# Kernel tuning notes

Hardware: AMD Instinct MI355X
Metric: run time of the kernel (lower is better)

Reference implementation:

```python
import jax, jax.numpy as jnp
import numpy as np
from jax import lax

B, C, D, H, W = 2, 64, 64, 96, 96
HID = 8  # max(C // 8, 8)
NEG_SLOPE = 0.01  # torch LeakyReLU default


def setup_inputs() -> dict:
    key = jax.random.key(0)
    k_x, k_dw, k_f1w, k_f1b, k_f2w, k_f2b = jax.random.split(key, 6)
    x = jax.random.normal(k_x, (B, C, D, H, W), dtype=jnp.float32)
    # depthwise 3x3x3 kernel, OIDHW with I = C/groups = 1
    dw_w = jax.random.normal(k_dw, (C, 1, 3, 3, 3), dtype=jnp.float32) * 0.2
    fc1_w = jax.random.normal(k_f1w, (HID, C), dtype=jnp.float32) * 0.1
    fc1_b = jax.random.normal(k_f1b, (HID,), dtype=jnp.float32) * 0.1
    fc2_w = jax.random.normal(k_f2w, (C, HID), dtype=jnp.float32) * 0.1
    fc2_b = jax.random.normal(k_f2b, (C,), dtype=jnp.float32) * 0.1
    return {"x": x, "dw_w": dw_w, "fc1_w": fc1_w, "fc1_b": fc1_b,
            "fc2_w": fc2_w, "fc2_b": fc2_b}


def reference(x, dw_w, fc1_w, fc1_b, fc2_w, fc2_b):
    # depthwise 3x3x3 conv, padding=1, groups=C
    s = lax.conv_general_dilated(
        x, dw_w,
        window_strides=(1, 1, 1),
        padding=[(1, 1), (1, 1), (1, 1)],
        dimension_numbers=("NCDHW", "OIDHW", "NCDHW"),
        feature_group_count=C,
    )
    # squeeze: global average pool over D,H,W -> [B, C]
    z = s.mean(axis=(2, 3, 4))
    # excitation MLP (1x1x1 convs on [B,C,1,1,1] == dense layers on [B,C])
    h = jnp.einsum("bc,hc->bh", z, fc1_w) + fc1_b
    h = jnp.where(h >= 0, h, NEG_SLOPE * h)  # LeakyReLU(0.01)
    w = jax.nn.sigmoid(jnp.einsum("bh,ch->bc", h, fc2_w) + fc2_b)
    # broadcast channel gate
    return x * w[:, :, None, None, None]
```

## Files before the change

kernel.cpp:

```cpp
#include <hip/hip_runtime.h>
#include <math.h>

#define B 2
#define C 64
#define DD 64
#define HH 96
#define WW 96
#define HID 8
#define BC (B * C)
#define SLICE (HH * WW)
#define SLICE4 (SLICE / 4)
#define CHAN (DD * SLICE)
#define CHAN4 (CHAN / 4)
#define ROW4 (WW / 4)

#define RED_BX 16
#define DPB (DD / RED_BX)
#define SC_F4 16
#define SC_BX (CHAN4 / (256 * SC_F4))

#define WS_PART 0
#define WS_CLS  (BC * RED_BX)
#define WS_GATE (WS_CLS + C * 27)

typedef float f4 __attribute__((ext_vector_type(4)));

__global__ void clsw_kernel(const float* __restrict__ dw_w, float* __restrict__ ws) {
    int c = blockIdx.x;
    int t = threadIdx.x;
    if (t < 27) {
        int cd = t / 9, r = t % 9, ch = r / 3, cw = r % 3;
        int kd0 = (cd == 2) ? 1 : 0, kd1 = (cd == 0) ? 1 : 2;
        int kh0 = (ch == 2) ? 1 : 0, kh1 = (ch == 0) ? 1 : 2;
        int kw0 = (cw == 2) ? 1 : 0, kw1 = (cw == 0) ? 1 : 2;
        float s = 0.f;
        for (int kd = kd0; kd <= kd1; ++kd)
            for (int kh = kh0; kh <= kh1; ++kh)
                for (int kw = kw0; kw <= kw1; ++kw)
                    s += dw_w[c * 27 + kd * 9 + kh * 3 + kw];
        ws[WS_CLS + c * 27 + t] = s;
    }
}

__global__ __launch_bounds__(256) void reduce_kernel(const float* __restrict__ x,
                                                     float* __restrict__ ws) {
    const int bc = blockIdx.y;
    const int c  = bc & (C - 1);
    const int d0 = blockIdx.x * DPB;
    const int tid = threadIdx.x;

    __shared__ float w9[9];
    __shared__ float part[4];

    const f4* xb = (const f4*)x + (size_t)bc * CHAN4;
    float acc = 0.f;

    const int h0 = tid / ROW4;
    const int j0 = tid - h0 * ROW4;

    for (int sd = 0; sd < DPB; ++sd) {
        const int d  = d0 + sd;
        const int cd = (d == 0) ? 0 : ((d == DD - 1) ? 2 : 1);
        __syncthreads();
        if (tid < 9) w9[tid] = ws[WS_CLS + c * 27 + cd * 9 + tid];
        __syncthreads();

        const f4* x4 = xb + (size_t)d * SLICE4;
        int h = h0, j = j0;
        #pragma unroll
        for (int it = 0; it < SLICE4 / 256; ++it) {
            f4 v = x4[it * 256 + tid];
            int chc = (h == 0) ? 0 : ((h == HH - 1) ? 2 : 1);
            float wmid = w9[chc * 3 + 1];
            float w0 = (j == 0) ? w9[chc * 3 + 0] : wmid;
            float w3 = (j == ROW4 - 1) ? w9[chc * 3 + 2] : wmid;
            acc += v.x * w0 + (v.y + v.z) * wmid + v.w * w3;
            h += 10; j += 16;
            if (j >= ROW4) { j -= ROW4; h += 1; }
        }
    }

    for (int off = 32; off > 0; off >>= 1)
        acc += __shfl_down(acc, off, 64);
    if ((tid & 63) == 0) part[tid >> 6] = acc;
    __syncthreads();
    if (tid == 0)
        ws[WS_PART + bc * RED_BX + blockIdx.x] = part[0] + part[1] + part[2] + part[3];
}

__global__ void gate_kernel(const float* __restrict__ fc1_w, const float* __restrict__ fc1_b,
                            const float* __restrict__ fc2_w, const float* __restrict__ fc2_b,
                            float* __restrict__ ws) {
    __shared__ float zsh[BC];
    __shared__ float hsh[B * HID];
    int t = threadIdx.x;
    float s0 = 0.f;
    for (int p = 0; p < RED_BX; ++p) s0 += ws[WS_PART + t * RED_BX + p];
    zsh[t] = s0 * (1.0f / (float)CHAN);
    __syncthreads();
    if (t < B * HID) {
        int b = t >> 3, j = t & 7;
        float s = fc1_b[j];
        for (int cc = 0; cc < C; ++cc) s += fc1_w[j * C + cc] * zsh[b * C + cc];
        hsh[t] = (s >= 0.f) ? s : 0.01f * s;
    }
    __syncthreads();
    int b = t >> 6, cc = t & (C - 1);
    float s = fc2_b[cc];
    for (int j = 0; j < HID; ++j) s += fc2_w[cc * HID + j] * hsh[b * HID + j];
    ws[WS_GATE + t] = 1.f / (1.f + expf(-s));
}

__global__ __launch_bounds__(256) void scale_kernel(const float* __restrict__ x,
                                                    const float* __restrict__ ws,
                                                    float* __restrict__ out) {
    const int bc = blockIdx.y;
    const float g = ws[WS_GATE + bc];
    const size_t base = (size_t)bc * CHAN4 + (size_t)blockIdx.x * (256 * SC_F4) + threadIdx.x;
    const f4* xp = (const f4*)x;
    f4* op = (f4*)out;
    #pragma unroll
    for (int k = 0; k < SC_F4; ++k) {
        size_t idx = base + (size_t)k * 256;
        f4 v = __builtin_nontemporal_load(&xp[idx]);
        f4 r = v * g;
        __builtin_nontemporal_store(r, &op[idx]);
    }
}

extern "C" void kernel_launch(void* const* d_in, const int* in_sizes, int n_in,
                              void* d_out, int out_size, void* d_ws, size_t ws_size,
                              hipStream_t stream) {
    const float* x     = (const float*)d_in[0];
    const float* dw_w  = (const float*)d_in[1];
    const float* fc1_w = (const float*)d_in[2];
    const float* fc1_b = (const float*)d_in[3];
    const float* fc2_w = (const float*)d_in[4];
    const float* fc2_b = (const float*)d_in[5];
    float* out = (float*)d_out;
    float* ws  = (float*)d_ws;

    clsw_kernel<<<dim3(C), dim3(64), 0, stream>>>(dw_w, ws);
    reduce_kernel<<<dim3(RED_BX, BC), dim3(256), 0, stream>>>(x, ws);
    gate_kernel<<<dim3(1), dim3(BC), 0, stream>>>(fc1_w, fc1_b, fc2_w, fc2_b, ws);
    scale_kernel<<<dim3(SC_BX, BC), dim3(256), 0, stream>>>(x, ws, out);
}
```

Before: 544.6 us.

## Fuse SE reduce, gate and scale into one cooperative persistent kernel

Replaces the four-kernel pipeline with a single cooperative kernel of 1024 blocks. Each block reduces its slab of x for both batches, waits at a grid-wide sync, computes the gate redundantly, then rescales the same slab in reverse order so the most recently read data may still be in cache. Edge-weight precompute moves into each block, and a non-cooperative fallback path is kept. This is meant to remove launch gaps and the second full read of x from HBM, at the cost of a grid barrier, redundant gate MLP work per block, and an occupancy requirement for co-residency.

```diff
diff --git a/kernel.cpp b/kernel.cpp
--- a/kernel.cpp
+++ b/kernel.cpp
@@ -1,4 +1,5 @@
 #include <hip/hip_runtime.h>
+#include <hip/hip_cooperative_groups.h>
 #include <math.h>
 
 #define B 2
@@ -14,22 +15,21 @@
 #define CHAN4 (CHAN / 4)
 #define ROW4 (WW / 4)
 
-#define RED_BX 16
-#define DPB (DD / RED_BX)
-#define SC_F4 16
-#define SC_BX (CHAN4 / (256 * SC_F4))
+#define NCHUNK 16
+#define DPB (DD / NCHUNK)
+#define GRID_BLK 1024
+#define ITERS (DPB * SLICE4 / 256)
 
 #define WS_PART 0
-#define WS_CLS  (BC * RED_BX)
-#define WS_GATE (WS_CLS + C * 27)
+#define WS_GATE (BC * NCHUNK)
 
 typedef float f4 __attribute__((ext_vector_type(4)));
-
-__global__ void clsw_kernel(const float* __restrict__ dw_w, float* __restrict__ ws) {
-    int c = blockIdx.x;
-    int t = threadIdx.x;
-    if (t < 27) {
-        int cd = t / 9, r = t % 9, ch = r / 3, cw = r % 3;
+namespace cg = cooperative_groups;
+
+__device__ __forceinline__ void compute_clsw(const float* __restrict__ dw_w,
+                                             int c, int tid, float* w27) {
+    if (tid < 27) {
+        int cd = tid / 9, r = tid % 9, ch = r / 3, cw = r % 3;
         int kd0 = (cd == 2) ? 1 : 0, kd1 = (cd == 0) ? 1 : 2;
         int kh0 = (ch == 2) ? 1 : 0, kh1 = (ch == 0) ? 1 : 2;
         int kw0 = (cw == 2) ? 1 : 0, kw1 = (cw == 0) ? 1 : 2;
@@ -38,34 +38,20 @@
             for (int kh = kh0; kh <= kh1; ++kh)
                 for (int kw = kw0; kw <= kw1; ++kw)
                     s += dw_w[c * 27 + kd * 9 + kh * 3 + kw];
-        ws[WS_CLS + c * 27 + t] = s;
-    }
-}
-
-__global__ __launch_bounds__(256) void reduce_kernel(const float* __restrict__ x,
-                                                     float* __restrict__ ws) {
-    const int bc = blockIdx.y;
-    const int c  = bc & (C - 1);
-    const int d0 = blockIdx.x * DPB;
-    const int tid = threadIdx.x;
-
-    __shared__ float w9[9];
-    __shared__ float part[4];
-
-    const f4* xb = (const f4*)x + (size_t)bc * CHAN4;
+        w27[tid] = s;
+    }
+}
+
+__device__ __forceinline__ float reduce_task(const float* __restrict__ x,
+                                             const float* w27,
+                                             int bc, int d0, int tid,
+                                             int h0, int j0) {
+    const f4* xb = (const f4*)x + (size_t)bc * CHAN4 + (size_t)d0 * SLICE4;
     float acc = 0.f;
-
-    const int h0 = tid / ROW4;
-    const int j0 = tid - h0 * ROW4;
-
     for (int sd = 0; sd < DPB; ++sd) {
-        const int d  = d0 + sd;
-        const int cd = (d == 0) ? 0 : ((d == DD - 1) ? 2 : 1);
-        __syncthreads();
-        if (tid < 9) w9[tid] = ws[WS_CLS + c * 27 + cd * 9 + tid];
-        __syncthreads();
-
-        const f4* x4 = xb + (size_t)d * SLICE4;
+        const int d = d0 + sd;
+        const float* w9 = &w27[((d == 0) ? 0 : ((d == DD - 1) ? 2 : 1)) * 9];
+        const f4* x4 = xb + (size_t)sd * SLICE4;
         int h = h0, j = j0;
         #pragma unroll
         for (int it = 0; it < SLICE4 / 256; ++it) {
@@ -79,23 +65,117 @@
             if (j >= ROW4) { j -= ROW4; h += 1; }
         }
     }
-
-    for (int off = 32; off > 0; off >>= 1)
-        acc += __shfl_down(acc, off, 64);
-    if ((tid & 63) == 0) part[tid >> 6] = acc;
-    __syncthreads();
-    if (tid == 0)
-        ws[WS_PART + bc * RED_BX + blockIdx.x] = part[0] + part[1] + part[2] + part[3];
-}
-
-__global__ void gate_kernel(const float* __restrict__ fc1_w, const float* __restrict__ fc1_b,
-                            const float* __restrict__ fc2_w, const float* __restrict__ fc2_b,
-                            float* __restrict__ ws) {
+    return acc;
+}
+
+__global__ __launch_bounds__(256, 4) void fused_se(
+        const float* __restrict__ x, const float* __restrict__ dw_w,
+        const float* __restrict__ fc1_w, const float* __restrict__ fc1_b,
+        const float* __restrict__ fc2_w, const float* __restrict__ fc2_b,
+        float* __restrict__ out, float* __restrict__ ws) {
+    const int tid   = threadIdx.x;
+    const int c     = blockIdx.x >> 4;
+    const int chunk = blockIdx.x & (NCHUNK - 1);
+    const int d0    = chunk * DPB;
+
+    __shared__ float w27[27];
+    __shared__ float part[4];
+    __shared__ float zsh[BC];
+    __shared__ float hsh[B * HID];
+    __shared__ float gsh[BC];
+
+    compute_clsw(dw_w, c, tid, w27);
+    __syncthreads();
+
+    const int h0 = tid / ROW4;
+    const int j0 = tid - h0 * ROW4;
+
+    for (int sel = 0; sel < 2; ++sel) {
+        const int bc = sel * C + c;
+        float acc = reduce_task(x, w27, bc, d0, tid, h0, j0);
+        for (int off = 32; off > 0; off >>= 1)
+            acc += __shfl_down(acc, off, 64);
+        __syncthreads();
+        if ((tid & 63) == 0) part[tid >> 6] = acc;
+        __syncthreads();
+        if (tid == 0)
+            ws[WS_PART + bc * NCHUNK + chunk] = part[0] + part[1] + part[2] + part[3];
+    }
+
+    __threadfence();
+    cg::this_grid().sync();
+
+    if (tid < BC) {
+        float s0 = 0.f;
+        #pragma unroll
+        for (int p = 0; p < NCHUNK; ++p) s0 += ws[WS_PART + tid * NCHUNK + p];
+        zsh[tid] = s0 * (1.0f / (float)CHAN);
+    }
+    __syncthreads();
+    if (tid < B * HID) {
+        int b = tid >> 3, j = tid & 7;
+        float s = fc1_b[j];
+        for (int cc = 0; cc < C; ++cc) s += fc1_w[j * C + cc] * zsh[b * C + cc];
+        hsh[tid] = (s >= 0.f) ? s : 0.01f * s;
+    }
+    __syncthreads();
+    if (tid < BC) {
+        int b = tid >> 6, cc = tid & (C - 1);
+        float s = fc2_b[cc];
+        for (int j = 0; j < HID; ++j) s += fc2_w[cc * HID + j] * hsh[b * HID + j];
+        gsh[tid] = 1.f / (1.f + expf(-s));
+    }
+    __syncthreads();
+
+    const f4* xp = (const f4*)x;
+    f4* op = (f4*)out;
+    for (int sel = 1; sel >= 0; --sel) {
+        const int bc = sel * C + c;
+        const float g = gsh[bc];
+        const size_t base = (size_t)bc * CHAN4 + (size_t)d0 * SLICE4 + tid;
+        #pragma unroll 6
+        for (int it = ITERS - 1; it >= 0; --it) {
+            size_t idx = base + (size_t)it * 256;
+            f4 v = xp[idx];
+            __builtin_nontemporal_store(v * g, &op[idx]);
+        }
+    }
+}
+
+__global__ __launch_bounds__(256) void fb_reduce(const float* __restrict__ x,
+                                                 const float* __restrict__ dw_w,
+                                                 float* __restrict__ ws) {
+    const int tid   = threadIdx.x;
+    const int c     = blockIdx.x >> 4;
+    const int chunk = blockIdx.x & (NCHUNK - 1);
+    const int d0    = chunk * DPB;
+    __shared__ float w27[27];
+    __shared__ float part[4];
+    compute_clsw(dw_w, c, tid, w27);
+    __syncthreads();
+    const int h0 = tid / ROW4;
+    const int j0 = tid - h0 * ROW4;
+    for (int sel = 0; sel < 2; ++sel) {
+        const int bc = sel * C + c;
+        float acc = reduce_task(x, w27, bc, d0, tid, h0, j0);
+        for (int off = 32; off > 0; off >>= 1)
+            acc += __shfl_down(acc, off, 64);
+        __syncthreads();
+        if ((tid & 63) == 0) part[tid >> 6] = acc;
+        __syncthreads();
+        if (tid == 0)
+            ws[WS_PART + bc * NCHUNK + chunk] = part[0] + part[1] + part[2] + part[3];
+    }
+}
+
+__global__ void fb_gate(const float* __restrict__ fc1_w, const float* __restrict__ fc1_b,
+                        const float* __restrict__ fc2_w, const float* __restrict__ fc2_b,
+                        float* __restrict__ ws) {
     __shared__ float zsh[BC];
     __shared__ float hsh[B * HID];
     int t = threadIdx.x;
     float s0 = 0.f;
-    for (int p = 0; p < RED_BX; ++p) s0 += ws[WS_PART + t * RED_BX + p];
+    for (int p = 0; p < NCHUNK; ++p) s0 += ws[WS_PART + t * NCHUNK + p];
     zsh[t] = s0 * (1.0f / (float)CHAN);
     __syncthreads();
     if (t < B * HID) {
@@ -111,20 +191,25 @@
     ws[WS_GATE + t] = 1.f / (1.f + expf(-s));
 }
 
-__global__ __launch_bounds__(256) void scale_kernel(const float* __restrict__ x,
-                                                    const float* __restrict__ ws,
-                                                    float* __restrict__ out) {
-    const int bc = blockIdx.y;
-    const float g = ws[WS_GATE + bc];
-    const size_t base = (size_t)bc * CHAN4 + (size_t)blockIdx.x * (256 * SC_F4) + threadIdx.x;
+__global__ __launch_bounds__(256) void fb_scale(const float* __restrict__ x,
+                                                const float* __restrict__ ws,
+                                                float* __restrict__ out) {
+    const int tid   = threadIdx.x;
+    const int c     = blockIdx.x >> 4;
+    const int chunk = blockIdx.x & (NCHUNK - 1);
+    const int d0    = chunk * DPB;
     const f4* xp = (const f4*)x;
     f4* op = (f4*)out;
-    #pragma unroll
-    for (int k = 0; k < SC_F4; ++k) {
-        size_t idx = base + (size_t)k * 256;
-        f4 v = __builtin_nontemporal_load(&xp[idx]);
-        f4 r = v * g;
-        __builtin_nontemporal_store(r, &op[idx]);
+    for (int sel = 1; sel >= 0; --sel) {
+        const int bc = sel * C + c;
+        const float g = ws[WS_GATE + bc];
+        const size_t base = (size_t)bc * CHAN4 + (size_t)d0 * SLICE4 + tid;
+        #pragma unroll 6
+        for (int it = ITERS - 1; it >= 0; --it) {
+            size_t idx = base + (size_t)it * 256;
+            f4 v = xp[idx];
+            __builtin_nontemporal_store(v * g, &op[idx]);
+        }
     }
 }
 
@@ -140,8 +225,13 @@
     float* out = (float*)d_out;
     float* ws  = (float*)d_ws;
 
-    clsw_kernel<<<dim3(C), dim3(64), 0, stream>>>(dw_w, ws);
-    reduce_kernel<<<dim3(RED_BX, BC), dim3(256), 0, stream>>>(x, ws);
-    gate_kernel<<<dim3(1), dim3(BC), 0, stream>>>(fc1_w, fc1_b, fc2_w, fc2_b, ws);
-    scale_kernel<<<dim3(SC_BX, BC), dim3(256), 0, stream>>>(x, ws, out);
-}
+    void* args[] = {(void*)&x, (void*)&dw_w, (void*)&fc1_w, (void*)&fc1_b,
+                    (void*)&fc2_w, (void*)&fc2_b, (void*)&out, (void*)&ws};
+    hipError_t e = hipLaunchCooperativeKernel(
+        reinterpret_cast<void*>(fused_se), dim3(GRID_BLK), dim3(256), args, 0, stream);
+    if (e != hipSuccess) {
+        fb_reduce<<<dim3(GRID_BLK), dim3(256), 0, stream>>>(x, dw_w, ws);
+        fb_gate<<<dim3(1), dim3(BC), 0, stream>>>(fc1_w, fc1_b, fc2_w, fc2_b, ws);
+        fb_scale<<<dim3(GRID_BLK), dim3(256), 0, stream>>>(x, ws, out);
+    }
+}
```

After: 863.8 us. +58.6%, slower.

## Fold weight-sum kernel into reduce, reverse scale order for cache reuse

Applied to the files above, without the earlier changes.

Removes the separate clsw kernel launch by having each reduce block compute the 27 boundary-class weight sums into shared memory once, which also drops the per-slice syncthreads pairs. The scale kernel now walks channels and blocks in reverse order and uses normal loads and stores instead of nontemporal ones. The intent is for the tail of x read last by the reduce pass to still be in the large last-level cache when scale starts. The cost is a redundant weight-sum computation in every reduce block and possible cache pollution from the ordinary stores.

```diff
diff --git a/kernel.cpp b/kernel.cpp
--- a/kernel.cpp
+++ b/kernel.cpp
@@ -20,16 +20,14 @@
 #define SC_BX (CHAN4 / (256 * SC_F4))
 
 #define WS_PART 0
-#define WS_CLS  (BC * RED_BX)
-#define WS_GATE (WS_CLS + C * 27)
+#define WS_GATE (BC * RED_BX)
 
 typedef float f4 __attribute__((ext_vector_type(4)));
 
-__global__ void clsw_kernel(const float* __restrict__ dw_w, float* __restrict__ ws) {
-    int c = blockIdx.x;
-    int t = threadIdx.x;
-    if (t < 27) {
-        int cd = t / 9, r = t % 9, ch = r / 3, cw = r % 3;
+__device__ __forceinline__ void compute_clsw(const float* __restrict__ dw_w,
+                                             int c, int tid, float* w27) {
+    if (tid < 27) {
+        int cd = tid / 9, r = tid % 9, ch = r / 3, cw = r % 3;
         int kd0 = (cd == 2) ? 1 : 0, kd1 = (cd == 0) ? 1 : 2;
         int kh0 = (ch == 2) ? 1 : 0, kh1 = (ch == 0) ? 1 : 2;
         int kw0 = (cw == 2) ? 1 : 0, kw1 = (cw == 0) ? 1 : 2;
@@ -38,19 +36,23 @@
             for (int kh = kh0; kh <= kh1; ++kh)
                 for (int kw = kw0; kw <= kw1; ++kw)
                     s += dw_w[c * 27 + kd * 9 + kh * 3 + kw];
-        ws[WS_CLS + c * 27 + t] = s;
+        w27[tid] = s;
     }
 }
 
 __global__ __launch_bounds__(256) void reduce_kernel(const float* __restrict__ x,
+                                                     const float* __restrict__ dw_w,
                                                      float* __restrict__ ws) {
     const int bc = blockIdx.y;
     const int c  = bc & (C - 1);
     const int d0 = blockIdx.x * DPB;
     const int tid = threadIdx.x;
 
-    __shared__ float w9[9];
+    __shared__ float w27[27];
     __shared__ float part[4];
+
+    compute_clsw(dw_w, c, tid, w27);
+    __syncthreads();
 
     const f4* xb = (const f4*)x + (size_t)bc * CHAN4;
     float acc = 0.f;
@@ -60,11 +62,7 @@
 
     for (int sd = 0; sd < DPB; ++sd) {
         const int d  = d0 + sd;
-        const int cd = (d == 0) ? 0 : ((d == DD - 1) ? 2 : 1);
-        __syncthreads();
-        if (tid < 9) w9[tid] = ws[WS_CLS + c * 27 + cd * 9 + tid];
-        __syncthreads();
-
+        const float* w9 = &w27[((d == 0) ? 0 : ((d == DD - 1) ? 2 : 1)) * 9];
         const f4* x4 = xb + (size_t)d * SLICE4;
         int h = h0, j = j0;
         #pragma unroll
@@ -114,17 +112,16 @@
 __global__ __launch_bounds__(256) void scale_kernel(const float* __restrict__ x,
                                                     const float* __restrict__ ws,
                                                     float* __restrict__ out) {
-    const int bc = blockIdx.y;
+    const int bc = (BC - 1) - blockIdx.y;
+    const int bx = (SC_BX - 1) - blockIdx.x;
     const float g = ws[WS_GATE + bc];
-    const size_t base = (size_t)bc * CHAN4 + (size_t)blockIdx.x * (256 * SC_F4) + threadIdx.x;
+    const size_t base = (size_t)bc * CHAN4 + (size_t)bx * (256 * SC_F4) + threadIdx.x;
     const f4* xp = (const f4*)x;
     f4* op = (f4*)out;
     #pragma unroll
     for (int k = 0; k < SC_F4; ++k) {
         size_t idx = base + (size_t)k * 256;
-        f4 v = __builtin_nontemporal_load(&xp[idx]);
-        f4 r = v * g;
-        __builtin_nontemporal_store(r, &op[idx]);
+        op[idx] = xp[idx] * g;
     }
 }
 
@@ -140,8 +137,7 @@
     float* out = (float*)d_out;
     float* ws  = (float*)d_ws;
 
-    clsw_kernel<<<dim3(C), dim3(64), 0, stream>>>(dw_w, ws);
-    reduce_kernel<<<dim3(RED_BX, BC), dim3(256), 0, stream>>>(x, ws);
+    reduce_kernel<<<dim3(RED_BX, BC), dim3(256), 0, stream>>>(x, dw_w, ws);
     gate_kernel<<<dim3(1), dim3(BC), 0, stream>>>(fc1_w, fc1_b, fc2_w, fc2_b, ws);
     scale_kernel<<<dim3(SC_BX, BC), dim3(256), 0, stream>>>(x, ws, out);
 }
```

Result: slower. 558.0 us (+2.5%).
